# Performance work log

Measured on AMD Instinct MI355X. Metric: run time of the kernel, lower is better.

Reference implementation:

```python
import jax, jax.numpy as jnp
import numpy as np

B, T, I, H, O = 64, 2048, 128, 256, 128


def setup_inputs() -> dict:
    key = jax.random.key(0)
    ks = jax.random.split(key, 7)
    s_xh = 1.0 / np.sqrt(I)
    s_hh = 1.0 / np.sqrt(H)
    return {
        "x": jax.random.normal(ks[0], (B, T, I), dtype=jnp.float32),
        "h0": jax.random.normal(ks[1], (B, H), dtype=jnp.float32),
        "Wxh": jax.random.uniform(ks[2], (H, I), jnp.float32, -s_xh, s_xh),
        "Whh": jax.random.uniform(ks[3], (H, H), jnp.float32, -s_hh, s_hh),
        "bh": jax.random.uniform(ks[4], (H,), jnp.float32, -s_hh, s_hh),
        "Wout": jax.random.uniform(ks[5], (O, H), jnp.float32, -s_hh, s_hh),
        "bout": jax.random.uniform(ks[6], (O,), jnp.float32, -s_hh, s_hh),
    }


def reference(x, h0, Wxh, Whh, bh, Wout, bout):
    # x: (B, T, I) -> scan over time with hidden state h: (B, H)
    def step(h, xt):
        # Elman cell: h' = tanh(x Wxh^T + h Whh^T + b)
        h_new = jnp.tanh(xt @ Wxh.T + h @ Whh.T + bh)
        y = h_new @ Wout.T + bout  # (B, O) per-step output head
        return h_new, y

    xT = jnp.swapaxes(x, 0, 1)  # (T, B, I)
    hT, Ys = jax.lax.scan(step, h0, xT)
    Y = jnp.swapaxes(Ys, 0, 1)  # (B, T, O)
    return Y, hT
```

## Files before the change

### kernel.cpp

```cpp
#include <hip/hip_runtime.h>
#include <hip/hip_bf16.h>
#include <hip/hip_fp16.h>

#define B_SZ 64
#define T_SZ 2048
#define I_SZ 128
#define H_SZ 256
#define O_SZ 128

typedef _Float16 half_t;
typedef _Float16 h2_t __attribute__((ext_vector_type(2)));
typedef __fp16   fp16x2_t __attribute__((ext_vector_type(2)));
typedef _Float16 h8_t __attribute__((ext_vector_type(8)));
typedef float    f4_t __attribute__((ext_vector_type(4)));

static __device__ __forceinline__ h2_t uint_as_h2(unsigned u) {
  union { unsigned u; h2_t h; } x; x.u = u; return x.h;
}
static __device__ __forceinline__ unsigned pack_h2(float a, float b) {
#if __has_builtin(__builtin_amdgcn_cvt_pkrtz)
  union { fp16x2_t h; unsigned u; } x;
  x.h = __builtin_amdgcn_cvt_pkrtz(a, b);
  return x.u;
#else
  h2_t h; h[0] = (_Float16)a; h[1] = (_Float16)b;
  union { h2_t h; unsigned u; } x2; x2.h = h; return x2.u;
#endif
}
static __device__ __forceinline__ float dot2(h2_t a, h2_t b, float c) {
#if __has_builtin(__builtin_amdgcn_fdot2)
  return __builtin_amdgcn_fdot2(a, b, c, false);
#else
  return c + (float)a[0] * (float)b[0] + (float)a[1] * (float)b[1];
#endif
}
static __device__ __forceinline__ float fast_rcp(float x) {
#if __has_builtin(__builtin_amdgcn_rcpf)
  return __builtin_amdgcn_rcpf(x);
#else
  return 1.0f / x;
#endif
}

template <int BM, int BN, int BK, int KTOT, bool A_HALF, bool OUT_HALF>
__global__ __launch_bounds__(256, 2) void gemm_tn_bias(
    const void* __restrict__ Ap, const float* __restrict__ Bw,
    const float* __restrict__ bias, void* __restrict__ Out, int ldo) {
  extern __shared__ half_t lds[];
  half_t* As = lds;
  half_t* Bs = lds + BM * BK;

  const int tid = threadIdx.x;
  const long row0 = (long)blockIdx.x * BM;
  const int col0 = blockIdx.y * BN;

  constexpr int MI = 4;
  constexpr int NJ = (BN / 2) / 16;
  const int lane = tid & 63, wid = tid >> 6;
  const int wm = (wid >> 1) * 64;
  const int wn = (wid & 1) * (BN / 2);

  f4_t acc[MI][NJ];
#pragma unroll
  for (int mi = 0; mi < MI; ++mi)
#pragma unroll
    for (int nj = 0; nj < NJ; ++nj) acc[mi][nj] = (f4_t){0.f, 0.f, 0.f, 0.f};

#pragma unroll 1
  for (int kt = 0; kt < KTOT / BK; ++kt) {
    if (kt) __syncthreads();
    constexpr int AIT = (BM * BK) / (256 * 8);
#pragma unroll
    for (int it = 0; it < AIT; ++it) {
      int idx = (it * 256 + tid) * 8;
      int r = idx / BK, c = idx % BK;
      uint4 v;
      if (A_HALF) {
        v = *(const uint4*)((const half_t*)Ap + (row0 + r) * (long)KTOT +
                            kt * BK + c);
      } else {
        const float* src =
            (const float*)Ap + (row0 + r) * (long)KTOT + kt * BK + c;
        float4 f0 = *(const float4*)(src);
        float4 f1 = *(const float4*)(src + 4);
        v.x = pack_h2(f0.x, f0.y); v.y = pack_h2(f0.z, f0.w);
        v.z = pack_h2(f1.x, f1.y); v.w = pack_h2(f1.z, f1.w);
      }
      int chunk = (c >> 3) ^ (r & 7);
      *(uint4*)(&As[r * BK + chunk * 8]) = v;
    }
    constexpr int BIT = (BN * BK) / (256 * 8);
#pragma unroll
    for (int it = 0; it < BIT; ++it) {
      int idx = (it * 256 + tid) * 8;
      int r = idx / BK, c = idx % BK;
      const float* src = Bw + (long)(col0 + r) * KTOT + kt * BK + c;
      float4 f0 = *(const float4*)(src);
      float4 f1 = *(const float4*)(src + 4);
      uint4 v;
      v.x = pack_h2(f0.x, f0.y); v.y = pack_h2(f0.z, f0.w);
      v.z = pack_h2(f1.x, f1.y); v.w = pack_h2(f1.z, f1.w);
      int chunk = (c >> 3) ^ (r & 7);
      *(uint4*)(&Bs[r * BK + chunk * 8]) = v;
    }
    __syncthreads();

#pragma unroll
    for (int ks = 0; ks < BK / 32; ++ks) {
      h8_t af[MI], bf[NJ];
#pragma unroll
      for (int mi = 0; mi < MI; ++mi) {
        int r = wm + mi * 16 + (lane & 15);
        int chunk = (ks * 4 + (lane >> 4)) ^ (r & 7);
        af[mi] = *(const h8_t*)(&As[r * BK + chunk * 8]);
      }
#pragma unroll
      for (int nj = 0; nj < NJ; ++nj) {
        int r = wn + nj * 16 + (lane & 15);
        int chunk = (ks * 4 + (lane >> 4)) ^ (r & 7);
        bf[nj] = *(const h8_t*)(&Bs[r * BK + chunk * 8]);
      }
#pragma unroll
      for (int mi = 0; mi < MI; ++mi)
#pragma unroll
        for (int nj = 0; nj < NJ; ++nj)
          acc[mi][nj] = __builtin_amdgcn_mfma_f32_16x16x32_f16(
              af[mi], bf[nj], acc[mi][nj], 0, 0, 0);
    }
  }

#pragma unroll
  for (int mi = 0; mi < MI; ++mi) {
#pragma unroll
    for (int nj = 0; nj < NJ; ++nj) {
#pragma unroll
      for (int e = 0; e < 4; ++e) {
        long row = row0 + wm + mi * 16 + (lane >> 4) * 4 + e;
        int col = col0 + wn + nj * 16 + (lane & 15);
        float val = acc[mi][nj][e] + bias[col];
        if (OUT_HALF)
          ((half_t*)Out)[row * ldo + col] = (half_t)val;
        else
          ((float*)Out)[row * ldo + col] = val;
      }
    }
  }
}

__global__ __launch_bounds__(512, 1) void rnn_scan(
    const half_t* __restrict__ Xp,
    const float* __restrict__ Whh,
    const float* __restrict__ h0,
    half_t* __restrict__ Hs,
    float* __restrict__ hT) {
  __shared__ __align__(16) unsigned short hbuf[2][H_SZ];
  const int tid = threadIdx.x;
  const int b = blockIdx.x;
  const int lane = tid & 63;
  const int w = tid >> 6;
  const int out = w * 32 + (lane >> 1);
  const int kh = lane & 1;

  unsigned wpk[64];
  {
    const float* wrow = Whh + out * H_SZ + kh * 128;
#pragma unroll
    for (int i = 0; i < 32; ++i) {
      float4 f = *(const float4*)(wrow + i * 4);
      wpk[2 * i] = pack_h2(f.x, f.y);
      wpk[2 * i + 1] = pack_h2(f.z, f.w);
    }
  }
  if (tid < H_SZ) {
    union { _Float16 h; unsigned short s; } cv;
    cv.h = (_Float16)h0[b * H_SZ + tid];
    hbuf[0][tid] = cv.s;
  }
  __syncthreads();

  const unsigned short* xp =
      (const unsigned short*)(Xp + (long)b * T_SZ * H_SZ + out);
  half_t* hs = Hs + (long)b * T_SZ * H_SZ + out;
  const bool writer = (kh == 0);

  unsigned short xr[8];
#pragma unroll
  for (int j = 0; j < 8; ++j) xr[j] = xp[(long)j * H_SZ];

#pragma unroll 1
  for (int tc = 0; tc < T_SZ; tc += 8) {
    unsigned short xn[8];
    const bool more = (tc + 8 < T_SZ);
#pragma unroll
    for (int j = 0; j < 8; ++j)
      xn[j] = more ? xp[(long)(tc + 8 + j) * H_SZ] : (unsigned short)0;

#pragma unroll
    for (int j = 0; j < 8; ++j) {
      const int t = tc + j;
      const int cur = t & 1;
      const uint4* hp = (const uint4*)(&hbuf[cur][kh * 128]);
      float a0 = 0.f, a1 = 0.f, a2 = 0.f, a3 = 0.f;
#pragma unroll
      for (int i = 0; i < 16; ++i) {
        uint4 v = hp[i];
        a0 = dot2(uint_as_h2(wpk[4 * i + 0]), uint_as_h2(v.x), a0);
        a1 = dot2(uint_as_h2(wpk[4 * i + 1]), uint_as_h2(v.y), a1);
        a2 = dot2(uint_as_h2(wpk[4 * i + 2]), uint_as_h2(v.z), a2);
        a3 = dot2(uint_as_h2(wpk[4 * i + 3]), uint_as_h2(v.w), a3);
      }
      float a = (a0 + a1) + (a2 + a3);
      a += __shfl_xor(a, 1);
      union { unsigned short s; _Float16 h; } xc; xc.s = xr[j];
      a += (float)xc.h;
      float ex = __expf(2.0f * a);
      float hn = 1.0f - 2.0f * fast_rcp(ex + 1.0f);

      if (writer) {
        union { _Float16 h; unsigned short s; } cv;
        cv.h = (_Float16)hn;
        hs[(long)t * H_SZ] = cv.h;
        hbuf[cur ^ 1][out] = cv.s;
        if (t == T_SZ - 1) hT[b * H_SZ + out] = hn;
      }
      __syncthreads();
    }
#pragma unroll
    for (int j = 0; j < 8; ++j) xr[j] = xn[j];
  }
}

extern "C" void kernel_launch(void* const* d_in, const int* in_sizes, int n_in,
                              void* d_out, int out_size, void* d_ws,
                              size_t ws_size, hipStream_t stream) {
  const float* x = (const float*)d_in[0];
  const float* h0 = (const float*)d_in[1];
  const float* Wxh = (const float*)d_in[2];
  const float* Whh = (const float*)d_in[3];
  const float* bh = (const float*)d_in[4];
  const float* Wout = (const float*)d_in[5];
  const float* bout = (const float*)d_in[6];

  half_t* Xp = (half_t*)d_out;
  half_t* Hs = (half_t*)d_ws;
  float* Y = (float*)d_out;
  float* hT = (float*)d_out + (long)B_SZ * T_SZ * O_SZ;

  const long M = (long)B_SZ * T_SZ;

  {
    dim3 grid((unsigned)(M / 128), H_SZ / 128);
    size_t sh = 2ull * 128 * 128 * sizeof(half_t);
    hipLaunchKernelGGL((gemm_tn_bias<128, 128, 128, 128, false, true>), grid,
                       dim3(256), sh, stream, (const void*)x, Wxh, bh,
                       (void*)Xp, H_SZ);
  }
  hipLaunchKernelGGL(rnn_scan, dim3(B_SZ), dim3(512), 0, stream, Xp, Whh, h0,
                     Hs, hT);
  {
    dim3 grid((unsigned)(M / 128), O_SZ / 128);
    size_t sh = 2ull * 128 * 128 * sizeof(half_t);
    hipLaunchKernelGGL((gemm_tn_bias<128, 128, 128, 256, true, false>), grid,
                       dim3(256), sh, stream, (const void*)Hs, Wout, bout,
                       (void*)Y, O_SZ);
  }
}
```

Measured before the change: 1.380 ms.

## Restructure RNN scan: 4 rows per 8-lane group with padded LDS and DPP reductions

Changes the recurrent scan's work split. Each group of 8 lanes now computes 4 output rows, and each lane covers a 32-element slice of K, so every LDS h-value read is reused for 4 rows instead of 1. The hidden-state buffer moves to a padded layout (80-byte stride per 32-element chunk) to avoid bank conflicts. The cross-lane reduction combines partial sums with DPP moves for xor 1 and 2 plus one shuffle for xor 4, folding 4 rows down to one per lane. The goal is to cut LDS read traffic and reduction latency on the serial critical path, at the cost of a deeper reduction tree and half the lanes idle at write-out.

```diff
diff --git a/kernel.cpp b/kernel.cpp
--- a/kernel.cpp
+++ b/kernel.cpp
@@ -39,6 +39,23 @@
   return __builtin_amdgcn_rcpf(x);
 #else
   return 1.0f / x;
+#endif
+}
+
+static __device__ __forceinline__ float dpp_add_xor1(float x) {
+#if __has_builtin(__builtin_amdgcn_mov_dpp)
+  int y = __builtin_amdgcn_mov_dpp(__float_as_int(x), 0xB1, 0xF, 0xF, true);
+  return x + __int_as_float(y);
+#else
+  return x + __shfl_xor(x, 1);
+#endif
+}
+static __device__ __forceinline__ float dpp_add_xor2(float x) {
+#if __has_builtin(__builtin_amdgcn_mov_dpp)
+  int y = __builtin_amdgcn_mov_dpp(__float_as_int(x), 0x4E, 0xF, 0xF, true);
+  return x + __int_as_float(y);
+#else
+  return x + __shfl_xor(x, 2);
 #endif
 }
 
@@ -153,35 +170,38 @@
     const float* __restrict__ h0,
     half_t* __restrict__ Hs,
     float* __restrict__ hT) {
-  __shared__ __align__(16) unsigned short hbuf[2][H_SZ];
+  __shared__ __align__(16) unsigned char hraw[2][8 * 80];
   const int tid = threadIdx.x;
   const int b = blockIdx.x;
   const int lane = tid & 63;
-  const int w = tid >> 6;
-  const int out = w * 32 + (lane >> 1);
-  const int kh = lane & 1;
-
-  unsigned wpk[64];
-  {
-    const float* wrow = Whh + out * H_SZ + kh * 128;
-#pragma unroll
-    for (int i = 0; i < 32; ++i) {
-      float4 f = *(const float4*)(wrow + i * 4);
-      wpk[2 * i] = pack_h2(f.x, f.y);
-      wpk[2 * i + 1] = pack_h2(f.z, f.w);
+  const int q = lane & 7;
+  const int g = tid >> 3;
+  const int orow = 4 * g + 2 * (q & 1) + ((q >> 1) & 1);
+  const bool writer = (q < 4);
+
+  unsigned wpk[4][16];
+#pragma unroll
+  for (int r = 0; r < 4; ++r) {
+    const float* wrow = Whh + (4 * g + r) * H_SZ + q * 32;
+#pragma unroll
+    for (int i = 0; i < 8; ++i) {
+      float4 f = *(const float4*)(wrow + 4 * i);
+      wpk[r][2 * i] = pack_h2(f.x, f.y);
+      wpk[r][2 * i + 1] = pack_h2(f.z, f.w);
     }
   }
   if (tid < H_SZ) {
     union { _Float16 h; unsigned short s; } cv;
     cv.h = (_Float16)h0[b * H_SZ + tid];
-    hbuf[0][tid] = cv.s;
+    *(unsigned short*)&hraw[0][(tid >> 5) * 80 + (tid & 31) * 2] = cv.s;
   }
   __syncthreads();
 
   const unsigned short* xp =
-      (const unsigned short*)(Xp + (long)b * T_SZ * H_SZ + out);
-  half_t* hs = Hs + (long)b * T_SZ * H_SZ + out;
-  const bool writer = (kh == 0);
+      (const unsigned short*)(Xp + (long)b * T_SZ * H_SZ + orow);
+  half_t* hs = Hs + (long)b * T_SZ * H_SZ + orow;
+  const int hwr_off = (orow >> 5) * 80 + (orow & 31) * 2;
+  const int hrd_off = q * 80;
 
   unsigned short xr[8];
 #pragma unroll
@@ -199,29 +219,40 @@
     for (int j = 0; j < 8; ++j) {
       const int t = tc + j;
       const int cur = t & 1;
-      const uint4* hp = (const uint4*)(&hbuf[cur][kh * 128]);
+      const uint4* hp = (const uint4*)(&hraw[cur][hrd_off]);
       float a0 = 0.f, a1 = 0.f, a2 = 0.f, a3 = 0.f;
 #pragma unroll
-      for (int i = 0; i < 16; ++i) {
+      for (int i = 0; i < 4; ++i) {
         uint4 v = hp[i];
-        a0 = dot2(uint_as_h2(wpk[4 * i + 0]), uint_as_h2(v.x), a0);
-        a1 = dot2(uint_as_h2(wpk[4 * i + 1]), uint_as_h2(v.y), a1);
-        a2 = dot2(uint_as_h2(wpk[4 * i + 2]), uint_as_h2(v.z), a2);
-        a3 = dot2(uint_as_h2(wpk[4 * i + 3]), uint_as_h2(v.w), a3);
-      }
-      float a = (a0 + a1) + (a2 + a3);
-      a += __shfl_xor(a, 1);
+#pragma unroll
+        for (int c = 0; c < 4; ++c) {
+          h2_t hh = uint_as_h2((&v.x)[c]);
+          a0 = dot2(uint_as_h2(wpk[0][4 * i + c]), hh, a0);
+          a1 = dot2(uint_as_h2(wpk[1][4 * i + c]), hh, a1);
+          a2 = dot2(uint_as_h2(wpk[2][4 * i + c]), hh, a2);
+          a3 = dot2(uint_as_h2(wpk[3][4 * i + c]), hh, a3);
+        }
+      }
+      float s0 = dpp_add_xor1(a0), s1 = dpp_add_xor1(a1);
+      float s2 = dpp_add_xor1(a2), s3 = dpp_add_xor1(a3);
+      float u0 = (q & 1) ? s2 : s0;
+      float u1 = (q & 1) ? s3 : s1;
+      u0 = dpp_add_xor2(u0);
+      u1 = dpp_add_xor2(u1);
+      float z = (q & 2) ? u1 : u0;
+      z += __shfl_xor(z, 4);
+
       union { unsigned short s; _Float16 h; } xc; xc.s = xr[j];
-      a += (float)xc.h;
-      float ex = __expf(2.0f * a);
+      z += (float)xc.h;
+      float ex = __expf(2.0f * z);
       float hn = 1.0f - 2.0f * fast_rcp(ex + 1.0f);
 
       if (writer) {
         union { _Float16 h; unsigned short s; } cv;
         cv.h = (_Float16)hn;
         hs[(long)t * H_SZ] = cv.h;
-        hbuf[cur ^ 1][out] = cv.s;
-        if (t == T_SZ - 1) hT[b * H_SZ + out] = hn;
+        *(unsigned short*)&hraw[cur ^ 1][hwr_off] = cv.s;
+        if (t == T_SZ - 1) hT[b * H_SZ + orow] = hn;
       }
       __syncthreads();
     }
```

Measured after the change: 1.148 ms. -16.8%, faster.
